# Kernel optimization log

Hardware: AMD Instinct MI355X
Metric: run time of the kernel (lower is better)

The kernel has to match this reference:

```python
import jax, jax.numpy as jnp
import numpy as np

B, S, K_DIM = 2, 2048, 2048
H, H_KV = 32, 8
HD = K_DIM // H  # 64
THETA = 10000.0


def apply_rope(x, position_ids, theta):
    # x: (B, H, S, hd), position_ids: (B, S) -- interleaved (even/odd) RoPE
    hd = x.shape[-1]
    dtype = x.dtype
    inv_freq = 1.0 / theta ** (jnp.arange(0, hd, 2, dtype=dtype) / hd)  # (hd/2,)
    freqs = position_ids.astype(dtype)[:, :, None] * inv_freq           # (B, S, hd/2)
    sin = jnp.sin(freqs)[:, None]  # (B, 1, S, hd/2)
    cos = jnp.cos(freqs)[:, None]
    x1 = x[..., ::2]
    x2 = x[..., 1::2]
    even = x1 * cos - x2 * sin
    odd = x2 * cos + x1 * sin
    return jnp.stack([even, odd], axis=-1).reshape(x.shape)


def setup_inputs() -> dict:
    key = jax.random.key(0)
    ks = jax.random.split(key, 5)
    x = jax.random.normal(ks[0], (B, S, K_DIM), dtype=jnp.float32)
    position_ids = jnp.broadcast_to(jnp.arange(S, dtype=jnp.int32)[None, :], (B, S))
    attention_mask = jnp.ones((B, S), dtype=jnp.int32)
    scale = 0.02
    Wq = jax.random.normal(ks[1], (H * HD, K_DIM), dtype=jnp.float32) * scale
    Wk = jax.random.normal(ks[2], (H_KV * HD, K_DIM), dtype=jnp.float32) * scale
    Wv = jax.random.normal(ks[3], (H_KV * HD, K_DIM), dtype=jnp.float32) * scale
    Wo = jax.random.normal(ks[4], (K_DIM, K_DIM), dtype=jnp.float32) * scale
    return {"x": x, "position_ids": position_ids, "attention_mask": attention_mask,
            "Wq": Wq, "Wk": Wk, "Wv": Wv, "Wo": Wo}


def reference(x, position_ids, attention_mask, Wq, Wk, Wv, Wo):
    b, s, kd = x.shape
    hd = HD
    q = (x @ Wq.T).reshape(b, s, H, hd).transpose(0, 2, 1, 3)     # (B, H, S, hd)
    k = (x @ Wk.T).reshape(b, s, H_KV, hd).transpose(0, 2, 1, 3)  # (B, Hkv, S, hd)
    v = (x @ Wv.T).reshape(b, s, H_KV, hd).transpose(0, 2, 1, 3)
    q = apply_rope(q, position_ids, THETA)
    k = apply_rope(k, position_ids, THETA)
    rep = H // H_KV
    # repeat_interleave over head dim == expand-within-group then flatten
    k = jnp.broadcast_to(k[:, :, None], (b, H_KV, rep, s, hd)).reshape(b, H, s, hd)
    v = jnp.broadcast_to(v[:, :, None], (b, H_KV, rep, s, hd)).reshape(b, H, s, hd)
    causal = jnp.triu(jnp.ones((s, s), dtype=bool), 1)            # True = masked
    pad = (attention_mask == 0)[:, None, None, :]                 # (B,1,1,S)
    mask = causal[None, None, :, :] | pad                         # (B,1,S,S) -> broadcast over H
    scores = jnp.einsum('bhqd,bhkd->bhqk', q, k) / jnp.sqrt(jnp.asarray(hd, x.dtype))
    scores = jnp.where(mask, jnp.finfo(scores.dtype).min, scores)
    attn = jax.nn.softmax(scores, axis=-1)
    out = jnp.einsum('bhqk,bhkd->bhqd', attn, v)
    out = out.transpose(0, 2, 1, 3).reshape(b, s, kd)
    return out @ Wo.T
```

## Files before the change

kernel.cpp:

```cpp
#include <hip/hip_runtime.h>
#include <hip/hip_bf16.h>

#define S_LEN 2048
#define BATCH 2
#define KDIM  2048
#define NH    32
#define NKV   8
#define HDIM  64

typedef short bf16s;
typedef short bf16x8 __attribute__((ext_vector_type(8)));
typedef short bf16x4 __attribute__((ext_vector_type(4)));
typedef float f32x4  __attribute__((ext_vector_type(4)));

#define KSCALE 0.1803368801111f

__device__ __forceinline__ bf16s f2bf(float f) {
  __hip_bfloat16 h = __float2bfloat16(f);
  return *reinterpret_cast<bf16s*>(&h);
}
__device__ __forceinline__ float ex2(float x) { return __builtin_amdgcn_exp2f(x); }

__device__ __forceinline__ void gload16(const void* g, void* l) {
  __builtin_amdgcn_global_load_lds(
      (const __attribute__((address_space(1))) char*)g,
      (__attribute__((address_space(3))) char*)l, 16, 0, 0);
}

__global__ void k_cvt(const float* __restrict__ src, bf16s* __restrict__ dst, int n) {
  int i = (blockIdx.x * blockDim.x + threadIdx.x) * 8;
  int stride = gridDim.x * blockDim.x * 8;
  for (; i < n; i += stride) {
    float4 a = *(const float4*)(src + i);
    float4 b = *(const float4*)(src + i + 4);
    bf16x8 o;
    o[0]=f2bf(a.x); o[1]=f2bf(a.y); o[2]=f2bf(a.z); o[3]=f2bf(a.w);
    o[4]=f2bf(b.x); o[5]=f2bf(b.y); o[6]=f2bf(b.z); o[7]=f2bf(b.w);
    *(bf16x8*)(dst + i) = o;
  }
}

__global__ void k_trig(float* __restrict__ qtab, float* __restrict__ ktab,
                       const int* __restrict__ pos) {
  const int idx = blockIdx.x * blockDim.x + threadIdx.x;
  if (idx >= S_LEN * 32) return;
  const int p = idx >> 5, i = idx & 31;
  const float inv = expf(-(float)(2 * i) * (1.0f / 64.0f) * 9.210340371976184f);
  const float fr = (float)p * inv;
  const float c = cosf(fr), s = sinf(fr);
  ktab[2 * idx]     = c;
  ktab[2 * idx + 1] = s;
  qtab[2 * idx]     = c * KSCALE;
  qtab[2 * idx + 1] = s * KSCALE;
}

__global__ __launch_bounds__(256, 2)
void k_gemm_qkv(const bf16s* __restrict__ A, const bf16s* __restrict__ Bw,
                const int* __restrict__ pos,
                const float* __restrict__ qtab, const float* __restrict__ ktab,
                bf16s* __restrict__ qb, bf16s* __restrict__ kb, bf16s* __restrict__ vtb) {
  const int K = KDIM;
  __shared__ bf16s As[128 * 32];
  __shared__ bf16s Bs[128 * 32];
  const int tid  = threadIdx.x;
  const int lane = tid & 63;
  const int w    = tid >> 6;
  const int wr   = w >> 1, wc = w & 1;
  const int l15  = lane & 15, lg = lane >> 4;
  const int by = blockIdx.y, bx = blockIdx.x;

  f32x4 acc[4][4] = {};

  const bf16s* gA0 = A  + (size_t)(by * 128 + (tid >> 2)) * K + ((tid & 3) << 3);
  const bf16s* gA1 = gA0 + (size_t)64 * K;
  const bf16s* gB0 = Bw + (size_t)(bx * 128 + (tid >> 2)) * K + ((tid & 3) << 3);
  const bf16s* gB1 = gB0 + (size_t)64 * K;
  bf16s* lA0 = &As[w * 512];
  bf16s* lA1 = &As[2048 + w * 512];
  bf16s* lB0 = &Bs[w * 512];
  bf16s* lB1 = &Bs[2048 + w * 512];

  const int nkt = K >> 5;
  for (int kt = 0; kt < nkt; ++kt) {
    __syncthreads();
    const int ko = kt << 5;
    gload16(gA0 + ko, lA0);
    gload16(gA1 + ko, lA1);
    gload16(gB0 + ko, lB0);
    gload16(gB1 + ko, lB1);
    __syncthreads();

    const bf16s* pa = &As[(wr * 64 + l15) * 32 + lg * 8];
    const bf16s* pb = &Bs[(wc * 64 + l15) * 32 + lg * 8];
    bf16x8 av[4], bv[4];
#pragma unroll
    for (int i = 0; i < 4; ++i) {
      av[i] = *(const bf16x8*)(pa + i * 512);
      bv[i] = *(const bf16x8*)(pb + i * 512);
    }
#pragma unroll
    for (int mi = 0; mi < 4; ++mi)
#pragma unroll
      for (int ni = 0; ni < 4; ++ni)
        acc[mi][ni] = __builtin_amdgcn_mfma_f32_16x16x32_bf16(av[mi], bv[ni], acc[mi][ni], 0, 0, 0);
  }

#pragma unroll
  for (int mi = 0; mi < 4; ++mi) {
    const int m0 = by * 128 + wr * 64 + mi * 16 + 4 * lg;
#pragma unroll
    for (int ni = 0; ni < 4; ++ni) {
      const int n = bx * 128 + wc * 64 + ni * 16 + l15;
      if (bx < 16) {
        const int d = n & 63, i = d >> 1;
        const float sgn = (d & 1) ? 1.f : -1.f;
#pragma unroll
        for (int r = 0; r < 4; ++r) {
          const int m = m0 + r;
          const float val = acc[mi][ni][r];
          const float par = __shfl_xor(val, 1);
          const float2 cs = *(const float2*)&qtab[((size_t)pos[m] << 6) + (i << 1)];
          qb[(size_t)m * KDIM + n] = f2bf(val * cs.x + sgn * par * cs.y);
        }
      } else if (bx < 20) {
        const int col = n - 2048;
        const int d = col & 63, i = d >> 1;
        const float sgn = (d & 1) ? 1.f : -1.f;
#pragma unroll
        for (int r = 0; r < 4; ++r) {
          const int m = m0 + r;
          const float val = acc[mi][ni][r];
          const float par = __shfl_xor(val, 1);
          const float2 cs = *(const float2*)&ktab[((size_t)pos[m] << 6) + (i << 1)];
          kb[(size_t)m * 512 + col] = f2bf(val * cs.x + sgn * par * cs.y);
        }
      } else {
        const int col = n - 2560;
        const int kvh = col >> 6, d = col & 63;
        const int b = m0 >> 11, s = m0 & (S_LEN - 1);
        bf16x4 pk;
#pragma unroll
        for (int r = 0; r < 4; ++r) pk[r] = f2bf(acc[mi][ni][r]);
        *(bf16x4*)&vtb[((size_t)((b * NKV + kvh) * HDIM + d)) * S_LEN + s] = pk;
      }
    }
  }
}

__global__ __launch_bounds__(256, 2)
void k_gemm_o(const bf16s* __restrict__ A, const bf16s* __restrict__ Bw,
              float* __restrict__ C, int N, int K) {
  __shared__ bf16s As[128 * 32];
  __shared__ bf16s Bs[128 * 32];
  const int tid  = threadIdx.x;
  const int lane = tid & 63;
  const int w    = tid >> 6;
  const int wr   = w >> 1, wc = w & 1;
  const int l15  = lane & 15, lg = lane >> 4;
  const int by = blockIdx.y, bx = blockIdx.x;

  f32x4 acc[4][4] = {};

  const bf16s* gA0 = A  + (size_t)(by * 128 + (tid >> 2)) * K + ((tid & 3) << 3);
  const bf16s* gA1 = gA0 + (size_t)64 * K;
  const bf16s* gB0 = Bw + (size_t)(bx * 128 + (tid >> 2)) * K + ((tid & 3) << 3);
  const bf16s* gB1 = gB0 + (size_t)64 * K;
  bf16s* lA0 = &As[w * 512];
  bf16s* lA1 = &As[2048 + w * 512];
  bf16s* lB0 = &Bs[w * 512];
  bf16s* lB1 = &Bs[2048 + w * 512];

  const int nkt = K >> 5;
  for (int kt = 0; kt < nkt; ++kt) {
    __syncthreads();
    const int ko = kt << 5;
    gload16(gA0 + ko, lA0);
    gload16(gA1 + ko, lA1);
    gload16(gB0 + ko, lB0);
    gload16(gB1 + ko, lB1);
    __syncthreads();

    const bf16s* pa = &As[(wr * 64 + l15) * 32 + lg * 8];
    const bf16s* pb = &Bs[(wc * 64 + l15) * 32 + lg * 8];
    bf16x8 av[4], bv[4];
#pragma unroll
    for (int i = 0; i < 4; ++i) {
      av[i] = *(const bf16x8*)(pa + i * 512);
      bv[i] = *(const bf16x8*)(pb + i * 512);
    }
#pragma unroll
    for (int mi = 0; mi < 4; ++mi)
#pragma unroll
      for (int ni = 0; ni < 4; ++ni)
        acc[mi][ni] = __builtin_amdgcn_mfma_f32_16x16x32_bf16(av[mi], bv[ni], acc[mi][ni], 0, 0, 0);
  }

#pragma unroll
  for (int mi = 0; mi < 4; ++mi) {
    const int m0 = by * 128 + wr * 64 + mi * 16 + 4 * lg;
#pragma unroll
    for (int ni = 0; ni < 4; ++ni) {
      const int n = bx * 128 + wc * 64 + ni * 16 + l15;
#pragma unroll
      for (int r = 0; r < 4; ++r)
        C[(size_t)(m0 + r) * N + n] = acc[mi][ni][r];
    }
  }
}

__global__ __launch_bounds__(256, 3)
void k_flash(const bf16s* __restrict__ q, const bf16s* __restrict__ k,
             const bf16s* __restrict__ vt, const int* __restrict__ amask,
             bf16s* __restrict__ out) {
  __shared__ bf16s Ks[2][64 * 64];
  __shared__ bf16s Vs[2][64 * 64];
  __shared__ bf16s Ps[4][32 * 64];

  const int tid = threadIdx.x, lane = tid & 63, w = tid >> 6;
  const int l15 = lane & 15, lg = lane >> 4;
  const int bh = blockIdx.x;
  const int y = blockIdx.y, yq = y & 3, hi = (y >> 3) & 1;
  const int qt = (y & 4) ? (yq + (hi << 2)) : ((hi ? 11 : 15) - yq);
  const int b = bh >> 5, h = bh & 31, kvh = h >> 2;
  const int nt = 2 * qt + 2;

  bf16x8 aq[2][2];
  const int qbase = qt * 128 + w * 32;
#pragma unroll
  for (int u = 0; u < 2; ++u) {
    const size_t qr = (size_t)(b * S_LEN + qbase + u * 16 + l15);
#pragma unroll
    for (int s = 0; s < 2; ++s)
      aq[u][s] = *(const bf16x8*)(q + qr * KDIM + h * HDIM + s * 32 + lg * 8);
  }

  const bf16s* kbase = k + (size_t)b * S_LEN * (NKV * HDIM) + kvh * HDIM;
  const bf16s* vbase = vt + ((size_t)(b * NKV + kvh) * HDIM) * S_LEN;

  const int srow0 = w * 16 + (lane >> 3);
  const int scol0 = (lane & 7) ^ (srow0 & 7);
  const int srow1 = srow0 + 8;
  const int scol1 = (lane & 7) ^ (srow1 & 7);

  auto stage = [&](int kt, int bufi) {
    gload16(kbase + (size_t)(kt * 64 + srow0) * (NKV * HDIM) + scol0 * 8, &Ks[bufi][w * 1024]);
    gload16(kbase + (size_t)(kt * 64 + srow1) * (NKV * HDIM) + scol1 * 8, &Ks[bufi][w * 1024 + 512]);
    gload16(vbase + (size_t)srow0 * S_LEN + kt * 64 + scol0 * 8, &Vs[bufi][w * 1024]);
    gload16(vbase + (size_t)srow1 * S_LEN + kt * 64 + scol1 * 8, &Vs[bufi][w * 1024 + 512]);
  };

  float m_run[2] = {-1e30f, -1e30f}, l_run[2] = {0.f, 0.f};
  f32x4 ao[2][4] = {};

  stage(0, 0);
  __syncthreads();

  int buf = 0;
  for (int kt = 0; kt < nt; ++kt) {
    if (kt + 1 < nt) stage(kt + 1, buf ^ 1);

    const unsigned long long bm = __ballot(amask[b * S_LEN + kt * 64 + lane] != 0);
    const bool allok = (bm == ~0ull);
    const bool diag = (kt >= nt - 2);

    f32x4 sc[2][4] = {};
#pragma unroll
    for (int c = 0; c < 4; ++c) {
      const int row = c * 16 + l15;
      const bf16s* kp = &Ks[buf][row * 64];
      const int xw = (row & 7) << 3;
      bf16x8 kb0 = *(const bf16x8*)(kp + ((lg * 8) ^ xw));
      bf16x8 kb1 = *(const bf16x8*)(kp + ((32 + lg * 8) ^ xw));
      sc[0][c] = __builtin_amdgcn_mfma_f32_16x16x32_bf16(kb0, aq[0][0], sc[0][c], 0, 0, 0);
      sc[0][c] = __builtin_amdgcn_mfma_f32_16x16x32_bf16(kb1, aq[0][1], sc[0][c], 0, 0, 0);
      sc[1][c] = __builtin_amdgcn_mfma_f32_16x16x32_bf16(kb0, aq[1][0], sc[1][c], 0, 0, 0);
      sc[1][c] = __builtin_amdgcn_mfma_f32_16x16x32_bf16(kb1, aq[1][1], sc[1][c], 0, 0, 0);
    }

#pragma unroll
    for (int u = 0; u < 2; ++u) {
      const int qg = qt * 128 + w * 32 + u * 16 + l15;
      float mt = -1e30f;
      if (diag || !allok) {
#pragma unroll
        for (int c = 0; c < 4; ++c)
#pragma unroll
          for (int r = 0; r < 4; ++r) {
            const int kg = kt * 64 + c * 16 + lg * 4 + r;
            float s = sc[u][c][r];
            if ((kg > qg) || (!allok && !((bm >> (kg & 63)) & 1))) s = -1e30f;
            sc[u][c][r] = s;
            mt = fmaxf(mt, s);
          }
      } else {
#pragma unroll
        for (int c = 0; c < 4; ++c)
#pragma unroll
          for (int r = 0; r < 4; ++r) mt = fmaxf(mt, sc[u][c][r]);
      }
      mt = fmaxf(mt, __shfl_xor(mt, 16));
      mt = fmaxf(mt, __shfl_xor(mt, 32));
      const float mn = fmaxf(m_run[u], mt);
      const float al = ex2(m_run[u] - mn);
      m_run[u] = mn;
      float ls = 0.f;
#pragma unroll
      for (int c = 0; c < 4; ++c) {
        bf16x4 pk;
#pragma unroll
        for (int r = 0; r < 4; ++r) {
          const float p = ex2(sc[u][c][r] - mn);
          ls += p;
          pk[r] = f2bf(p);
        }
        const int prow = u * 16 + l15;
        *(bf16x4*)&Ps[w][prow * 64 + ((c * 16 + lg * 4) ^ ((prow & 7) << 3))] = pk;
      }
      ls += __shfl_xor(ls, 16);
      ls += __shfl_xor(ls, 32);
      l_run[u] = l_run[u] * al + ls;
#pragma unroll
      for (int vc = 0; vc < 4; ++vc)
#pragma unroll
        for (int r = 0; r < 4; ++r) ao[u][vc][r] *= al;
    }

    bf16x8 pa[2][2];
#pragma unroll
    for (int u = 0; u < 2; ++u) {
      const int prow = u * 16 + l15;
      const int px = (prow & 7) << 3;
#pragma unroll
      for (int s = 0; s < 2; ++s)
        pa[u][s] = *(const bf16x8*)&Ps[w][prow * 64 + ((s * 32 + lg * 8) ^ px)];
    }

#pragma unroll
    for (int vc = 0; vc < 4; ++vc) {
      const int row = vc * 16 + l15;
      const bf16s* vp = &Vs[buf][row * 64];
      const int xw = (row & 7) << 3;
      bf16x8 vb0 = *(const bf16x8*)(vp + ((lg * 8) ^ xw));
      bf16x8 vb1 = *(const bf16x8*)(vp + ((32 + lg * 8) ^ xw));
      ao[0][vc] = __builtin_amdgcn_mfma_f32_16x16x32_bf16(vb0, pa[0][0], ao[0][vc], 0, 0, 0);
      ao[0][vc] = __builtin_amdgcn_mfma_f32_16x16x32_bf16(vb1, pa[0][1], ao[0][vc], 0, 0, 0);
      ao[1][vc] = __builtin_amdgcn_mfma_f32_16x16x32_bf16(vb0, pa[1][0], ao[1][vc], 0, 0, 0);
      ao[1][vc] = __builtin_amdgcn_mfma_f32_16x16x32_bf16(vb1, pa[1][1], ao[1][vc], 0, 0, 0);
    }

    __syncthreads();
    buf ^= 1;
  }

#pragma unroll
  for (int u = 0; u < 2; ++u) {
    const float inv = 1.0f / l_run[u];
    const size_t m = (size_t)b * S_LEN + qt * 128 + w * 32 + u * 16 + l15;
#pragma unroll
    for (int vc = 0; vc < 4; ++vc) {
      bf16x4 ov;
#pragma unroll
      for (int r = 0; r < 4; ++r) ov[r] = f2bf(ao[u][vc][r] * inv);
      *(bf16x4*)&out[m * KDIM + h * HDIM + vc * 16 + lg * 4] = ov;
    }
  }
}

extern "C" void kernel_launch(void* const* d_in, const int* in_sizes, int n_in,
                              void* d_out, int out_size, void* d_ws, size_t ws_size,
                              hipStream_t stream) {
  const float* x  = (const float*)d_in[0];
  const int* pos  = (const int*)d_in[1];
  const int* am   = (const int*)d_in[2];
  const float* Wq = (const float*)d_in[3];
  const float* Wk = (const float*)d_in[4];
  const float* Wv = (const float*)d_in[5];
  const float* Wo = (const float*)d_in[6];
  float* out = (float*)d_out;

  char* ws = (char*)d_ws;
  const int M = BATCH * S_LEN;
  bf16s* xb   = (bf16s*)(ws);
  bf16s* wqkv = (bf16s*)(ws + 16777216);
  bf16s* wob  = (bf16s*)(ws + 29360128);
  bf16s* qb   = (bf16s*)(ws + 37748736);
  bf16s* kb   = (bf16s*)(ws + 54525952);
  bf16s* vtb  = (bf16s*)(ws + 58720256);
  bf16s* aob  = (bf16s*)(ws + 62914560);
  float* qtab = (float*)(ws + 62914560);
  float* ktab = (float*)(ws + 63438848);

  dim3 blk(256);
  auto cvt = [&](const float* s, bf16s* d, int n) {
    int g = (n / 8 + 255) / 256; if (g > 2048) g = 2048;
    k_cvt<<<dim3(g), blk, 0, stream>>>(s, d, n);
  };
  cvt(x,  xb,  M * KDIM);
  cvt(Wq, wqkv,               2048 * 2048);
  cvt(Wk, wqkv + 2048 * 2048,  512 * 2048);
  cvt(Wv, wqkv + 2560 * 2048,  512 * 2048);
  cvt(Wo, wob, 2048 * 2048);

  k_trig<<<dim3((S_LEN * 32 + 255) / 256), blk, 0, stream>>>(qtab, ktab, pos);

  k_gemm_qkv<<<dim3(24, 32), blk, 0, stream>>>(xb, wqkv, pos, qtab, ktab, qb, kb, vtb);

  k_flash<<<dim3(BATCH * NH, S_LEN / 128), blk, 0, stream>>>(qb, kb, vtb, am, aob);

  k_gemm_o<<<dim3(16, 32), blk, 0, stream>>>(aob, wob, out, 2048, 2048);
}
```

Measured before the change: 206.5 us.

## Merge conversion launches, skip redundant softmax rescale, raise MFMA priority

The five fp32-to-bf16 conversion launches become one kernel that picks its source by element range and writes into the contiguous workspace, which relies on xb, wqkv and wob lying back to back. In the flash loop, the running-max update and the rescaling of the accumulator and l are skipped when no lane's tile max exceeds the running max. s_setprio is raised around both MFMA blocks so those waves are scheduled ahead of others. The gains are fewer launches and less VALU work per tile, at the cost of a wave-wide vote and a branch.

```diff
diff --git a/kernel.cpp b/kernel.cpp
--- a/kernel.cpp
+++ b/kernel.cpp
@@ -27,16 +27,26 @@
       (__attribute__((address_space(3))) char*)l, 16, 0, 0);
 }
 
-__global__ void k_cvt(const float* __restrict__ src, bf16s* __restrict__ dst, int n) {
-  int i = (blockIdx.x * blockDim.x + threadIdx.x) * 8;
-  int stride = gridDim.x * blockDim.x * 8;
-  for (; i < n; i += stride) {
-    float4 a = *(const float4*)(src + i);
-    float4 b = *(const float4*)(src + i + 4);
+__global__ void k_cvt_all(const float* __restrict__ s0, const float* __restrict__ s1,
+                          const float* __restrict__ s2, const float* __restrict__ s3,
+                          const float* __restrict__ s4, bf16s* __restrict__ dst) {
+  const int NU = 2359296;
+  int u = blockIdx.x * blockDim.x + threadIdx.x;
+  const int stride = gridDim.x * blockDim.x;
+  for (; u < NU; u += stride) {
+    const int e = u * 8;
+    const float* src; int off;
+    if (e < 8388608)       { src = s0; off = e; }
+    else if (e < 12582912) { src = s1; off = e - 8388608; }
+    else if (e < 13631488) { src = s2; off = e - 12582912; }
+    else if (e < 14680064) { src = s3; off = e - 13631488; }
+    else                   { src = s4; off = e - 14680064; }
+    float4 a = *(const float4*)(src + off);
+    float4 b = *(const float4*)(src + off + 4);
     bf16x8 o;
     o[0]=f2bf(a.x); o[1]=f2bf(a.y); o[2]=f2bf(a.z); o[3]=f2bf(a.w);
     o[4]=f2bf(b.x); o[5]=f2bf(b.y); o[6]=f2bf(b.z); o[7]=f2bf(b.w);
-    *(bf16x8*)(dst + i) = o;
+    *(bf16x8*)(dst + e) = o;
   }
 }
 
@@ -264,6 +274,7 @@
     const bool diag = (kt >= nt - 2);
 
     f32x4 sc[2][4] = {};
+    __builtin_amdgcn_s_setprio(1);
 #pragma unroll
     for (int c = 0; c < 4; ++c) {
       const int row = c * 16 + l15;
@@ -276,6 +287,7 @@
       sc[1][c] = __builtin_amdgcn_mfma_f32_16x16x32_bf16(kb0, aq[1][0], sc[1][c], 0, 0, 0);
       sc[1][c] = __builtin_amdgcn_mfma_f32_16x16x32_bf16(kb1, aq[1][1], sc[1][c], 0, 0, 0);
     }
+    __builtin_amdgcn_s_setprio(0);
 
 #pragma unroll
     for (int u = 0; u < 2; ++u) {
@@ -300,16 +312,24 @@
       }
       mt = fmaxf(mt, __shfl_xor(mt, 16));
       mt = fmaxf(mt, __shfl_xor(mt, 32));
-      const float mn = fmaxf(m_run[u], mt);
-      const float al = ex2(m_run[u] - mn);
-      m_run[u] = mn;
+      if (!__all(mt <= m_run[u])) {
+        const float mn = fmaxf(m_run[u], mt);
+        const float al = ex2(m_run[u] - mn);
+        m_run[u] = mn;
+        l_run[u] *= al;
+#pragma unroll
+        for (int vc = 0; vc < 4; ++vc)
+#pragma unroll
+          for (int r = 0; r < 4; ++r) ao[u][vc][r] *= al;
+      }
+      const float mb = m_run[u];
       float ls = 0.f;
 #pragma unroll
       for (int c = 0; c < 4; ++c) {
         bf16x4 pk;
 #pragma unroll
         for (int r = 0; r < 4; ++r) {
-          const float p = ex2(sc[u][c][r] - mn);
+          const float p = ex2(sc[u][c][r] - mb);
           ls += p;
           pk[r] = f2bf(p);
         }
@@ -318,11 +338,7 @@
       }
       ls += __shfl_xor(ls, 16);
       ls += __shfl_xor(ls, 32);
-      l_run[u] = l_run[u] * al + ls;
-#pragma unroll
-      for (int vc = 0; vc < 4; ++vc)
-#pragma unroll
-        for (int r = 0; r < 4; ++r) ao[u][vc][r] *= al;
+      l_run[u] += ls;
     }
 
     bf16x8 pa[2][2];
@@ -335,6 +351,7 @@
         pa[u][s] = *(const bf16x8*)&Ps[w][prow * 64 + ((s * 32 + lg * 8) ^ px)];
     }
 
+    __builtin_amdgcn_s_setprio(1);
 #pragma unroll
     for (int vc = 0; vc < 4; ++vc) {
       const int row = vc * 16 + l15;
@@ -347,6 +364,7 @@
       ao[1][vc] = __builtin_amdgcn_mfma_f32_16x16x32_bf16(vb0, pa[1][0], ao[1][vc], 0, 0, 0);
       ao[1][vc] = __builtin_amdgcn_mfma_f32_16x16x32_bf16(vb1, pa[1][1], ao[1][vc], 0, 0, 0);
     }
+    __builtin_amdgcn_s_setprio(0);
 
     __syncthreads();
     buf ^= 1;
@@ -391,15 +409,8 @@
   float* ktab = (float*)(ws + 63438848);
 
   dim3 blk(256);
-  auto cvt = [&](const float* s, bf16s* d, int n) {
-    int g = (n / 8 + 255) / 256; if (g > 2048) g = 2048;
-    k_cvt<<<dim3(g), blk, 0, stream>>>(s, d, n);
-  };
-  cvt(x,  xb,  M * KDIM);
-  cvt(Wq, wqkv,               2048 * 2048);
-  cvt(Wk, wqkv + 2048 * 2048,  512 * 2048);
-  cvt(Wv, wqkv + 2560 * 2048,  512 * 2048);
-  cvt(Wo, wob, 2048 * 2048);
+
+  k_cvt_all<<<dim3(2048), blk, 0, stream>>>(x, Wq, Wk, Wv, Wo, xb);
 
   k_trig<<<dim3((S_LEN * 32 + 255) / 256), blk, 0, stream>>>(qtab, ktab, pos);
 
```

New measurement: 199.7 us. -3.3%, faster.
